# Kernel tuning notes

Hardware: AMD Instinct MI355X
Metric: run time of the kernel (lower is better)

Reference implementation:

```python
import jax, jax.numpy as jnp
import numpy as np
import math

IN_DIM = 512
OUT_DIM = 512
MOD_DIM = 512
B, S = 4, 4096
EPS = 1e-8


def setup_inputs() -> dict:
    key = jax.random.key(0)
    k1, k2, k3, k4 = jax.random.split(key, 4)
    x = jax.random.normal(k1, (B, S, IN_DIM), dtype=jnp.float32)
    modulation = jax.random.normal(k2, (B, S, MOD_DIM), dtype=jnp.float32)
    # main weight: kaiming_normal_(a=0.2, fan_in, leaky_relu) -> std = sqrt(2/(1+0.2^2)) / sqrt(in_dim)
    gain = math.sqrt(2.0 / (1.0 + 0.2 ** 2))
    weight = gain / math.sqrt(IN_DIM) * jax.random.normal(k3, (OUT_DIM, IN_DIM), dtype=jnp.float32)
    bias = jnp.zeros((OUT_DIM,), dtype=jnp.float32)
    # modulation Linear: cips_bias_init -> weight ~ N(0, 1/sqrt(fan_in)), bias = 1.0
    mod_w = (1.0 / math.sqrt(MOD_DIM)) * jax.random.normal(k4, (IN_DIM, MOD_DIM), dtype=jnp.float32)
    mod_b = jnp.ones((IN_DIM,), dtype=jnp.float32)
    return {"x": x, "modulation": modulation, "weight": weight, "bias": bias,
            "mod_w": mod_w, "mod_b": mod_b}


def reference(x, modulation, weight, bias, mod_w, mod_b):
    # s = modulation linear -> per-token scale on input features  [B,S,in]
    s = jnp.einsum('bsm,im->bsi', modulation, mod_w) + mod_b
    # Algebraic rewrite of StyleGAN2 modulated linear (same math, never
    # materializes [B,S,out,in]):
    #   out[b,s,o] = sum_i (W[o,i]*s[b,s,i]*demod[b,s,o]) * x[b,s,i]
    #             = demod[b,s,o] * sum_i W[o,i] * (s*x)[b,s,i]
    #   demod = rsqrt(sum_i (W[o,i]*s[b,s,i])^2 + eps)
    out = jnp.einsum('bsi,oi->bso', x * s, weight)
    demod = jax.lax.rsqrt(jnp.einsum('bsi,oi->bso', s * s, weight * weight) + EPS)
    # torch computes demod under no_grad -> constant; irrelevant for fwd but kept explicit
    out = out * jax.lax.stop_gradient(demod) + bias
    return out
```

## Files before the change

### kernel.cpp

```cpp
#include <hip/hip_runtime.h>
#include <hip/hip_bf16.h>


#define T_TOK 16384
#define DIM 512

typedef __attribute__((ext_vector_type(4))) float f32x4;
typedef __attribute__((ext_vector_type(8))) short bf16x8;

static __device__ __forceinline__ unsigned short f2bf(float f) {
    union { float f; unsigned int u; } v; v.f = f;
    unsigned int u = v.u;
    u += 0x7fffu + ((u >> 16) & 1u);
    return (unsigned short)(u >> 16);
}
static __device__ __forceinline__ float bf2f(unsigned short h) {
    union { unsigned int u; float f; } v; v.u = ((unsigned int)h) << 16;
    return v.f;
}

__global__ __launch_bounds__(256) void k0_convert(
    const float* __restrict__ mod, const float* __restrict__ weight,
    const float* __restrict__ mod_w,
    unsigned short* __restrict__ modb, unsigned short* __restrict__ Wb,
    unsigned short* __restrict__ W2b, unsigned short* __restrict__ mwb)
{
    const int NV_MOD = (T_TOK * DIM) / 4;
    const int NV_W   = (DIM * DIM) / 4;
    int idx = blockIdx.x * blockDim.x + threadIdx.x;
    int stride = gridDim.x * blockDim.x;
    for (int i = idx; i < NV_MOD; i += stride) {
        f32x4 v = ((const f32x4*)mod)[i];
        ushort4 o; o.x = f2bf(v[0]); o.y = f2bf(v[1]); o.z = f2bf(v[2]); o.w = f2bf(v[3]);
        ((ushort4*)modb)[i] = o;
    }
    for (int i = idx; i < NV_W; i += stride) {
        f32x4 v = ((const f32x4*)weight)[i];
        ushort4 o;  o.x = f2bf(v[0]); o.y = f2bf(v[1]); o.z = f2bf(v[2]); o.w = f2bf(v[3]);
        ((ushort4*)Wb)[i] = o;
        ushort4 o2; o2.x = f2bf(v[0]*v[0]); o2.y = f2bf(v[1]*v[1]);
                    o2.z = f2bf(v[2]*v[2]); o2.w = f2bf(v[3]*v[3]);
        ((ushort4*)W2b)[i] = o2;
        f32x4 m = ((const f32x4*)mod_w)[i];
        ushort4 o3; o3.x = f2bf(m[0]); o3.y = f2bf(m[1]); o3.z = f2bf(m[2]); o3.w = f2bf(m[3]);
        ((ushort4*)mwb)[i] = o3;
    }
}


__global__ __launch_bounds__(256, 2) void k1_style(
    const unsigned short* __restrict__ modb,
    const unsigned short* __restrict__ mwb,
    const float* __restrict__ x,
    const float* __restrict__ mod_b,
    unsigned short* __restrict__ xs,
    unsigned short* __restrict__ ss)
{
    __shared__ union {
        struct { unsigned short A[128 * 64]; unsigned short B[128 * 64]; } stg;
        unsigned short str[128 * 144];
    } u;
    const int tid  = threadIdx.x;
    const int lane = tid & 63;
    const int w    = tid >> 6;
    const int wr   = w >> 1, wc = w & 1;
    const int nbn  = DIM / 128;
    const int bm   = blockIdx.x / nbn;
    const int bn   = blockIdx.x % nbn;

    const int srow  = lane >> 3;
    const int lslot = (lane & 7) ^ srow;
    const int fr    = lane & 15;
    const int fs    = lane >> 4;

    f32x4 acc[4][4] = {};

    const size_t aBase = (size_t)bm * 128 * DIM;
    const size_t bBase = (size_t)bn * 128 * DIM;

    for (int kb = 0; kb < DIM; kb += 64) {
#pragma unroll
        for (int q = 0; q < 4; ++q) {
            int row = w * 32 + q * 8 + srow;
            const unsigned short* ga = modb + aBase + (size_t)row * DIM + kb + lslot * 8;
            const unsigned short* gb = mwb  + bBase + (size_t)row * DIM + kb + lslot * 8;
            __builtin_amdgcn_global_load_lds(
                (__attribute__((address_space(1))) void*)ga,
                (__attribute__((address_space(3))) void*)(u.stg.A + w * 2048 + q * 512), 16, 0, 0);
            __builtin_amdgcn_global_load_lds(
                (__attribute__((address_space(1))) void*)gb,
                (__attribute__((address_space(3))) void*)(u.stg.B + w * 2048 + q * 512), 16, 0, 0);
        }
        __syncthreads();
#pragma unroll
        for (int kk = 0; kk < 64; kk += 32) {
            bf16x8 af[4], bfv[4];
#pragma unroll
            for (int mi = 0; mi < 4; ++mi) {
                int row = wr * 64 + mi * 16 + fr;
                int ps  = ((kk >> 3) + fs) ^ (fr & 7);
                af[mi] = *(const bf16x8*)(u.stg.A + row * 64 + ps * 8);
            }
#pragma unroll
            for (int ni = 0; ni < 4; ++ni) {
                int row = wc * 64 + ni * 16 + fr;
                int ps  = ((kk >> 3) + fs) ^ (fr & 7);
                bfv[ni] = *(const bf16x8*)(u.stg.B + row * 64 + ps * 8);
            }
#pragma unroll
            for (int mi = 0; mi < 4; ++mi)
#pragma unroll
                for (int ni = 0; ni < 4; ++ni)
                    acc[mi][ni] = __builtin_amdgcn_mfma_f32_16x16x32_bf16(
                        af[mi], bfv[ni], acc[mi][ni], 0, 0, 0);
        }
        __syncthreads();
    }

#pragma unroll
    for (int ni = 0; ni < 4; ++ni) {
        int col = wc * 64 + ni * 16 + fr;
        float mb = mod_b[bn * 128 + col];
#pragma unroll
        for (int mi = 0; mi < 4; ++mi) {
#pragma unroll
            for (int j = 0; j < 4; ++j) {
                int row = wr * 64 + mi * 16 + fs * 4 + j;
                u.str[row * 144 + col] = f2bf(acc[mi][ni][j] + mb);
            }
        }
    }
    __syncthreads();
#pragma unroll
    for (int q = 0; q < 8; ++q) {
        int row = w * 32 + q * 4 + (lane >> 4);
        int c8  = (lane & 15) * 8;
        bf16x8 s8 = *(const bf16x8*)(u.str + row * 144 + c8);
        size_t off = ((size_t)bm * 128 + row) * DIM + bn * 128 + c8;
        f32x4 x0 = *(const f32x4*)(x + off);
        f32x4 x1 = *(const f32x4*)(x + off + 4);
        bf16x8 xsv, ssv;
#pragma unroll
        for (int e = 0; e < 8; ++e) {
            float sf = bf2f((unsigned short)s8[e]);
            float xv = (e < 4) ? x0[e] : x1[e - 4];
            xsv[e] = (short)f2bf(xv * sf);
            ssv[e] = (short)f2bf(sf * sf);
        }
        *(bf16x8*)(xs + off) = xsv;
        *(bf16x8*)(ss + off) = ssv;
    }
}

__global__ __launch_bounds__(256, 2) void k2_main(
    const unsigned short* __restrict__ xs,
    const unsigned short* __restrict__ ss,
    const unsigned short* __restrict__ Wb,
    const unsigned short* __restrict__ W2b,
    const float* __restrict__ bias,
    float* __restrict__ out)
{
    __shared__ unsigned short lXS[128 * 64];
    __shared__ unsigned short lSS[128 * 64];
    __shared__ unsigned short lW [128 * 64];
    __shared__ unsigned short lW2[128 * 64];
    const int tid  = threadIdx.x;
    const int lane = tid & 63;
    const int w    = tid >> 6;
    const int wr   = w >> 1, wc = w & 1;
    const int nbn  = DIM / 128;
    const int bm   = blockIdx.x / nbn;
    const int bn   = blockIdx.x % nbn;

    const int srow  = lane >> 3;
    const int lslot = (lane & 7) ^ srow;
    const int fr    = lane & 15;
    const int fs    = lane >> 4;

    f32x4 a1[4][4] = {};
    f32x4 a2[4][4] = {};

    const size_t aBase = (size_t)bm * 128 * DIM;
    const size_t bBase = (size_t)bn * 128 * DIM;

    for (int kb = 0; kb < DIM; kb += 64) {
#pragma unroll
        for (int q = 0; q < 4; ++q) {
            int row = w * 32 + q * 8 + srow;
            size_t goffA = aBase + (size_t)row * DIM + kb + lslot * 8;
            size_t goffB = bBase + (size_t)row * DIM + kb + lslot * 8;
            unsigned ldso = w * 2048 + q * 512;
            __builtin_amdgcn_global_load_lds(
                (__attribute__((address_space(1))) void*)(xs + goffA),
                (__attribute__((address_space(3))) void*)(lXS + ldso), 16, 0, 0);
            __builtin_amdgcn_global_load_lds(
                (__attribute__((address_space(1))) void*)(ss + goffA),
                (__attribute__((address_space(3))) void*)(lSS + ldso), 16, 0, 0);
            __builtin_amdgcn_global_load_lds(
                (__attribute__((address_space(1))) void*)(Wb + goffB),
                (__attribute__((address_space(3))) void*)(lW + ldso), 16, 0, 0);
            __builtin_amdgcn_global_load_lds(
                (__attribute__((address_space(1))) void*)(W2b + goffB),
                (__attribute__((address_space(3))) void*)(lW2 + ldso), 16, 0, 0);
        }
        __syncthreads();
#pragma unroll
        for (int kk = 0; kk < 64; kk += 32) {
            bf16x8 axs[4], ass[4], bw[4], bw2[4];
#pragma unroll
            for (int mi = 0; mi < 4; ++mi) {
                int row = wr * 64 + mi * 16 + fr;
                int ps  = ((kk >> 3) + fs) ^ (fr & 7);
                axs[mi] = *(const bf16x8*)(lXS + row * 64 + ps * 8);
                ass[mi] = *(const bf16x8*)(lSS + row * 64 + ps * 8);
            }
#pragma unroll
            for (int ni = 0; ni < 4; ++ni) {
                int row = wc * 64 + ni * 16 + fr;
                int ps  = ((kk >> 3) + fs) ^ (fr & 7);
                bw[ni]  = *(const bf16x8*)(lW  + row * 64 + ps * 8);
                bw2[ni] = *(const bf16x8*)(lW2 + row * 64 + ps * 8);
            }
#pragma unroll
            for (int mi = 0; mi < 4; ++mi)
#pragma unroll
                for (int ni = 0; ni < 4; ++ni) {
                    a1[mi][ni] = __builtin_amdgcn_mfma_f32_16x16x32_bf16(
                        axs[mi], bw[ni], a1[mi][ni], 0, 0, 0);
                    a2[mi][ni] = __builtin_amdgcn_mfma_f32_16x16x32_bf16(
                        ass[mi], bw2[ni], a2[mi][ni], 0, 0, 0);
                }
        }
        __syncthreads();
    }

#pragma unroll
    for (int ni = 0; ni < 4; ++ni) {
        int o = bn * 128 + wc * 64 + ni * 16 + fr;
        float bo = bias[o];
#pragma unroll
        for (int mi = 0; mi < 4; ++mi) {
#pragma unroll
            for (int j = 0; j < 4; ++j) {
                size_t t = (size_t)bm * 128 + wr * 64 + mi * 16 + fs * 4 + j;
                float d = rsqrtf(a2[mi][ni][j] + 1e-8f);
                out[t * DIM + o] = a1[mi][ni][j] * d + bo;
            }
        }
    }
}

extern "C" void kernel_launch(void* const* d_in, const int* in_sizes, int n_in,
                              void* d_out, int out_size, void* d_ws, size_t ws_size,
                              hipStream_t stream) {
    const float* x      = (const float*)d_in[0];
    const float* mod    = (const float*)d_in[1];
    const float* weight = (const float*)d_in[2];
    const float* bias   = (const float*)d_in[3];
    const float* mod_w  = (const float*)d_in[4];
    const float* mod_b  = (const float*)d_in[5];
    float* out = (float*)d_out;

    char* ws = (char*)d_ws;
    unsigned short* modb = (unsigned short*)(ws);
    unsigned short* xs   = (unsigned short*)(ws + (size_t)16777216);
    unsigned short* ssb  = (unsigned short*)(ws + (size_t)2 * 16777216);
    unsigned short* Wb   = (unsigned short*)(ws + (size_t)3 * 16777216);
    unsigned short* W2b  = (unsigned short*)(ws + (size_t)3 * 16777216 + 524288);
    unsigned short* mwb  = (unsigned short*)(ws + (size_t)3 * 16777216 + 2 * 524288);

    hipLaunchKernelGGL(k0_convert, dim3(2048), dim3(256), 0, stream,
                       mod, weight, mod_w, modb, Wb, W2b, mwb);
    hipLaunchKernelGGL(k1_style, dim3(512), dim3(256), 0, stream,
                       modb, mwb, x, mod_b, xs, ssb);
    hipLaunchKernelGGL(k2_main, dim3(512), dim3(256), 0, stream,
                       xs, ssb, Wb, W2b, bias, out);
}
```

Before: 61.27 us.

## Shrink main GEMM tile to 64x128, stage output through LDS, remap block order

```diff
diff --git a/kernel.cpp b/kernel.cpp
--- a/kernel.cpp
+++ b/kernel.cpp
@@ -48,7 +48,7 @@
 }
 
 
-__global__ __launch_bounds__(256, 2) void k1_style(
+__global__ __launch_bounds__(256, 4) void k1_style(
     const unsigned short* __restrict__ modb,
     const unsigned short* __restrict__ mwb,
     const float* __restrict__ x,
@@ -64,9 +64,9 @@
     const int lane = tid & 63;
     const int w    = tid >> 6;
     const int wr   = w >> 1, wc = w & 1;
-    const int nbn  = DIM / 128;
-    const int bm   = blockIdx.x / nbn;
-    const int bn   = blockIdx.x % nbn;
+    const int tile = (blockIdx.x & 7) * 64 + (blockIdx.x >> 3);
+    const int bm   = tile >> 2;
+    const int bn   = tile & 3;
 
     const int srow  = lane >> 3;
     const int lslot = (lane & 7) ^ srow;
@@ -152,7 +152,7 @@
     }
 }
 
-__global__ __launch_bounds__(256, 2) void k2_main(
+__global__ __launch_bounds__(256, 3) void k2_main(
     const unsigned short* __restrict__ xs,
     const unsigned short* __restrict__ ss,
     const unsigned short* __restrict__ Wb,
@@ -160,69 +160,78 @@
     const float* __restrict__ bias,
     float* __restrict__ out)
 {
-    __shared__ unsigned short lXS[128 * 64];
-    __shared__ unsigned short lSS[128 * 64];
-    __shared__ unsigned short lW [128 * 64];
-    __shared__ unsigned short lW2[128 * 64];
+    __shared__ union {
+        struct {
+            unsigned short XS[64 * 64];
+            unsigned short SS[64 * 64];
+            unsigned short W [128 * 64];
+            unsigned short W2[128 * 64];
+        } stg;
+        float tr[64 * 132];
+    } u;
     const int tid  = threadIdx.x;
     const int lane = tid & 63;
     const int w    = tid >> 6;
-    const int wr   = w >> 1, wc = w & 1;
-    const int nbn  = DIM / 128;
-    const int bm   = blockIdx.x / nbn;
-    const int bn   = blockIdx.x % nbn;
+    const int tile = (blockIdx.x & 7) * 128 + (blockIdx.x >> 3);
+    const int bm   = tile >> 2;
+    const int bn   = tile & 3;
 
     const int srow  = lane >> 3;
     const int lslot = (lane & 7) ^ srow;
     const int fr    = lane & 15;
     const int fs    = lane >> 4;
 
-    f32x4 a1[4][4] = {};
-    f32x4 a2[4][4] = {};
-
-    const size_t aBase = (size_t)bm * 128 * DIM;
+    f32x4 a1[2][4] = {};
+    f32x4 a2[2][4] = {};
+
+    const size_t aBase = (size_t)bm * 64 * DIM;
     const size_t bBase = (size_t)bn * 128 * DIM;
 
     for (int kb = 0; kb < DIM; kb += 64) {
 #pragma unroll
+        for (int q = 0; q < 2; ++q) {
+            int rowb = (w * 2 + q) * 8;
+            int row  = rowb + srow;
+            size_t ga = aBase + (size_t)row * DIM + kb + lslot * 8;
+            __builtin_amdgcn_global_load_lds(
+                (__attribute__((address_space(1))) void*)(xs + ga),
+                (__attribute__((address_space(3))) void*)(u.stg.XS + rowb * 64), 16, 0, 0);
+            __builtin_amdgcn_global_load_lds(
+                (__attribute__((address_space(1))) void*)(ss + ga),
+                (__attribute__((address_space(3))) void*)(u.stg.SS + rowb * 64), 16, 0, 0);
+        }
+#pragma unroll
         for (int q = 0; q < 4; ++q) {
-            int row = w * 32 + q * 8 + srow;
-            size_t goffA = aBase + (size_t)row * DIM + kb + lslot * 8;
-            size_t goffB = bBase + (size_t)row * DIM + kb + lslot * 8;
-            unsigned ldso = w * 2048 + q * 512;
-            __builtin_amdgcn_global_load_lds(
-                (__attribute__((address_space(1))) void*)(xs + goffA),
-                (__attribute__((address_space(3))) void*)(lXS + ldso), 16, 0, 0);
-            __builtin_amdgcn_global_load_lds(
-                (__attribute__((address_space(1))) void*)(ss + goffA),
-                (__attribute__((address_space(3))) void*)(lSS + ldso), 16, 0, 0);
-            __builtin_amdgcn_global_load_lds(
-                (__attribute__((address_space(1))) void*)(Wb + goffB),
-                (__attribute__((address_space(3))) void*)(lW + ldso), 16, 0, 0);
-            __builtin_amdgcn_global_load_lds(
-                (__attribute__((address_space(1))) void*)(W2b + goffB),
-                (__attribute__((address_space(3))) void*)(lW2 + ldso), 16, 0, 0);
+            int rowb = (w * 4 + q) * 8;
+            int row  = rowb + srow;
+            size_t gb = bBase + (size_t)row * DIM + kb + lslot * 8;
+            __builtin_amdgcn_global_load_lds(
+                (__attribute__((address_space(1))) void*)(Wb + gb),
+                (__attribute__((address_space(3))) void*)(u.stg.W + rowb * 64), 16, 0, 0);
+            __builtin_amdgcn_global_load_lds(
+                (__attribute__((address_space(1))) void*)(W2b + gb),
+                (__attribute__((address_space(3))) void*)(u.stg.W2 + rowb * 64), 16, 0, 0);
         }
         __syncthreads();
 #pragma unroll
         for (int kk = 0; kk < 64; kk += 32) {
-            bf16x8 axs[4], ass[4], bw[4], bw2[4];
-#pragma unroll
-            for (int mi = 0; mi < 4; ++mi) {
-                int row = wr * 64 + mi * 16 + fr;
-                int ps  = ((kk >> 3) + fs) ^ (fr & 7);
-                axs[mi] = *(const bf16x8*)(lXS + row * 64 + ps * 8);
-                ass[mi] = *(const bf16x8*)(lSS + row * 64 + ps * 8);
+            bf16x8 axs[2], ass[2], bw[4], bw2[4];
+#pragma unroll
+            for (int mi = 0; mi < 2; ++mi) {
+                int row = (w >> 1) * 32 + mi * 16 + fr;
+                int ps  = ((kk >> 3) + fs) ^ (fr & 7);
+                axs[mi] = *(const bf16x8*)(u.stg.XS + row * 64 + ps * 8);
+                ass[mi] = *(const bf16x8*)(u.stg.SS + row * 64 + ps * 8);
             }
 #pragma unroll
             for (int ni = 0; ni < 4; ++ni) {
-                int row = wc * 64 + ni * 16 + fr;
-                int ps  = ((kk >> 3) + fs) ^ (fr & 7);
-                bw[ni]  = *(const bf16x8*)(lW  + row * 64 + ps * 8);
-                bw2[ni] = *(const bf16x8*)(lW2 + row * 64 + ps * 8);
-            }
-#pragma unroll
-            for (int mi = 0; mi < 4; ++mi)
+                int row = (w & 1) * 64 + ni * 16 + fr;
+                int ps  = ((kk >> 3) + fs) ^ (fr & 7);
+                bw[ni]  = *(const bf16x8*)(u.stg.W  + row * 64 + ps * 8);
+                bw2[ni] = *(const bf16x8*)(u.stg.W2 + row * 64 + ps * 8);
+            }
+#pragma unroll
+            for (int mi = 0; mi < 2; ++mi)
 #pragma unroll
                 for (int ni = 0; ni < 4; ++ni) {
                     a1[mi][ni] = __builtin_amdgcn_mfma_f32_16x16x32_bf16(
@@ -236,17 +245,26 @@
 
 #pragma unroll
     for (int ni = 0; ni < 4; ++ni) {
-        int o = bn * 128 + wc * 64 + ni * 16 + fr;
-        float bo = bias[o];
-#pragma unroll
-        for (int mi = 0; mi < 4; ++mi) {
+        int col = (w & 1) * 64 + ni * 16 + fr;
+        float bo = bias[bn * 128 + col];
+#pragma unroll
+        for (int mi = 0; mi < 2; ++mi) {
 #pragma unroll
             for (int j = 0; j < 4; ++j) {
-                size_t t = (size_t)bm * 128 + wr * 64 + mi * 16 + fs * 4 + j;
+                int row = (w >> 1) * 32 + mi * 16 + fs * 4 + j;
                 float d = rsqrtf(a2[mi][ni][j] + 1e-8f);
-                out[t * DIM + o] = a1[mi][ni][j] * d + bo;
-            }
-        }
+                u.tr[row * 132 + col] = a1[mi][ni][j] * d + bo;
+            }
+        }
+    }
+    __syncthreads();
+    {
+        int r  = tid >> 2;
+        int c0 = (tid & 3) * 32;
+        size_t ob = ((size_t)bm * 64 + r) * DIM + bn * 128 + c0;
+#pragma unroll
+        for (int k = 0; k < 8; ++k)
+            *(f32x4*)(out + ob + 4 * k) = *(const f32x4*)(u.tr + r * 132 + c0 + 4 * k);
     }
 }
 
@@ -273,6 +291,6 @@
                        mod, weight, mod_w, modb, Wb, W2b, mwb);
     hipLaunchKernelGGL(k1_style, dim3(512), dim3(256), 0, stream,
                        modb, mwb, x, mod_b, xs, ssb);
-    hipLaunchKernelGGL(k2_main, dim3(512), dim3(256), 0, stream,
+    hipLaunchKernelGGL(k2_main, dim3(1024), dim3(256), 0, stream,
                        xs, ssb, Wb, W2b, bias, out);
 }
```

Result: slower. 93.40 us (+52.4%).
